# Kernel optimization log

Hardware: AMD Instinct MI355X
Metric: run time of the kernel (lower is better)

Reference implementation:

```python
import jax, jax.numpy as jnp
import numpy as np

B, S, D, H = 4, 4096, 2048, 512
EPS = 1e-5


def setup_inputs() -> dict:
    key = jax.random.key(0)
    ks = jax.random.split(key, 5)
    x = jax.random.normal(ks[0], (B, S, D), dtype=jnp.float32)
    ln_gamma = jnp.ones((D,), dtype=jnp.float32)
    ln_beta = jnp.zeros((D,), dtype=jnp.float32)
    # 'small' init: uniform in [1e-5 - 1e-6, 1e-5 + 1e-6]; use scaled randn here
    # so gradients are non-trivial, same math either way.
    W_down = jax.random.normal(ks[1], (H, D), dtype=jnp.float32) * 0.02
    b_down = jax.random.normal(ks[2], (H,), dtype=jnp.float32) * 0.02
    W_up = jax.random.normal(ks[3], (D, H), dtype=jnp.float32) * 0.02
    b_up = jax.random.normal(ks[4], (D,), dtype=jnp.float32) * 0.02
    return {"x": x, "ln_gamma": ln_gamma, "ln_beta": ln_beta,
            "W_down": W_down, "b_down": b_down, "W_up": W_up, "b_up": b_up}


def _layer_norm(x, gamma, beta):
    mu = jnp.mean(x, axis=-1, keepdims=True)
    var = jnp.mean(jnp.square(x - mu), axis=-1, keepdims=True)
    return (x - mu) * jax.lax.rsqrt(var + EPS) * gamma + beta


def reference(x, ln_gamma, ln_beta, W_down, b_down, W_up, b_up):
    # LayerNorm -> down-proj -> ReLU -> up-proj -> residual add
    y = _layer_norm(x, ln_gamma, ln_beta)                      # [B,S,D]
    y = jnp.einsum('bsd,hd->bsh', y, W_down) + b_down          # [B,S,H]
    y = jax.nn.relu(y)
    y = jnp.einsum('bsh,dh->bsd', y, W_up) + b_up              # [B,S,D]
    return x + y
```

## Files before the change

kernel.cpp:

```cpp
#include <hip/hip_runtime.h>

#define DD 2048
#define HH 512
#define NTOK 16384

typedef __attribute__((ext_vector_type(8))) short short8_t;
typedef __attribute__((ext_vector_type(4))) short short4_t;
typedef __attribute__((ext_vector_type(4))) float f32x4;

static __device__ __forceinline__ short f2bf(float f) {
    union { float f; unsigned u; } v; v.f = f;
    unsigned r = (v.u + 0x7fffu + ((v.u >> 16) & 1u)) >> 16;
    return (short)r;
}
static __device__ __forceinline__ float bf2f(unsigned short s) {
    union { unsigned u; float f; } v; v.u = (unsigned)s << 16;
    return v.f;
}

static __device__ __forceinline__ void gl16(const short* g, short* l) {
    __builtin_amdgcn_global_load_lds(
        (const __attribute__((address_space(1))) unsigned int*)g,
        (__attribute__((address_space(3))) unsigned int*)l, 16, 0, 0);
}

__global__ __launch_bounds__(256) void k_prep(
    const float* __restrict__ Wd, const float* __restrict__ g,
    const float* __restrict__ be, const float* __restrict__ Wu,
    const float* __restrict__ x,
    short* __restrict__ Wg, short* __restrict__ Wub,
    float* __restrict__ c2, short* __restrict__ xn,
    float* __restrict__ muv, float* __restrict__ sdv)
{
    __shared__ float ss[4], sq[4];
    int bid = blockIdx.x;
    int w = threadIdx.x >> 6, lane = threadIdx.x & 63;
    if (bid < 128) {
        int h = bid * 4 + w;
        const float* wr = Wd + (size_t)h * DD;
        float s2 = 0.f;
        for (int i = 0; i < 8; i++) {
            int col = i * 256 + lane * 4;
            float4 wv = *(const float4*)(wr + col);
            float4 gv = *(const float4*)(g + col);
            float4 bv = *(const float4*)(be + col);
            s2 += bv.x * wv.x + bv.y * wv.y + bv.z * wv.z + bv.w * wv.w;
            short4_t o;
            o[0] = f2bf(wv.x * gv.x); o[1] = f2bf(wv.y * gv.y);
            o[2] = f2bf(wv.z * gv.z); o[3] = f2bf(wv.w * gv.w);
            *(short4_t*)(Wg + (size_t)h * DD + col) = o;
        }
        for (int m = 1; m < 64; m <<= 1) s2 += __shfl_xor(s2, m);
        if (lane == 0) c2[h] = s2;
    } else if (bid < 384) {
        int b = bid - 128;
        for (int r = 0; r < 4; r++) {
            int i = (b * 4 + r) * 1024 + threadIdx.x * 4;
            float4 v = *(const float4*)(Wu + i);
            short4_t o;
            o[0] = f2bf(v.x); o[1] = f2bf(v.y); o[2] = f2bf(v.z); o[3] = f2bf(v.w);
            *(short4_t*)(Wub + i) = o;
        }
    } else {
        int row = bid - 384;
        const float* xr = x + (size_t)row * DD + threadIdx.x * 8;
        float4 a = *(const float4*)xr;
        float4 b = *(const float4*)(xr + 4);
        float s = a.x + a.y + a.z + a.w + b.x + b.y + b.z + b.w;
        float q = a.x * a.x + a.y * a.y + a.z * a.z + a.w * a.w
                + b.x * b.x + b.y * b.y + b.z * b.z + b.w * b.w;
        for (int m = 1; m < 64; m <<= 1) { s += __shfl_xor(s, m); q += __shfl_xor(q, m); }
        if (lane == 0) { ss[w] = s; sq[w] = q; }
        __syncthreads();
        float S = ss[0] + ss[1] + ss[2] + ss[3];
        float Q = sq[0] + sq[1] + sq[2] + sq[3];
        float mu = S * (1.f / DD);
        float ve = Q * (1.f / DD) - mu * mu + 1e-5f;
        float rs = rsqrtf(ve);
        if (threadIdx.x == 0) { muv[row] = mu; sdv[row] = ve * rs; }
        short8_t o;
        o[0] = f2bf((a.x - mu) * rs); o[1] = f2bf((a.y - mu) * rs);
        o[2] = f2bf((a.z - mu) * rs); o[3] = f2bf((a.w - mu) * rs);
        o[4] = f2bf((b.x - mu) * rs); o[5] = f2bf((b.y - mu) * rs);
        o[6] = f2bf((b.z - mu) * rs); o[7] = f2bf((b.w - mu) * rs);
        *(short8_t*)(xn + (size_t)row * DD + threadIdx.x * 8) = o;
    }
}

__global__ __launch_bounds__(256, 2) void k_down(
    const short* __restrict__ xn, const short* __restrict__ Wg,
    const float* __restrict__ c2, const float* __restrict__ bd,
    short* __restrict__ hid)
{
    __shared__ __align__(16) short sA[2][128 * 64];
    __shared__ __align__(16) short sB[2][128 * 64];

    int bid = blockIdx.x;
    int nb = (bid & 7) * 64 + (bid >> 3);
    const int m0 = (nb >> 2) * 128;
    const int n0 = (nb & 3) * 128;

    const int tid = threadIdx.x, lane = tid & 63, w = tid >> 6;
    const int l15 = lane & 15, rg = lane >> 4;
    const int wm = w >> 1, wn = w & 1;

    auto stage = [&](int b, int kb) {
#pragma unroll
        for (int i = 0; i < 4; i++) {
            int ch = i * 256 + tid;
            int r = ch >> 3, c = ch & 7;
            int co = ((c ^ (r & 7)) << 3);
            gl16(xn + (size_t)(m0 + r) * DD + kb + co,
                 &sA[b][0] + (i * 256 + (w << 6)) * 8);
            gl16(Wg + (size_t)(n0 + r) * DD + kb + co,
                 &sB[b][0] + (i * 256 + (w << 6)) * 8);
        }
    };

    f32x4 acc[4][4];
#pragma unroll
    for (int i = 0; i < 4; i++)
#pragma unroll
        for (int j = 0; j < 4; j++) acc[i][j] = (f32x4){0.f, 0.f, 0.f, 0.f};

    stage(0, 0);
    __syncthreads();

    for (int t = 0; t < 32; t++) {
        int cur = t & 1, nxt = cur ^ 1;
        if (t < 31) stage(nxt, (t + 1) * 64);
#pragma unroll
        for (int kk = 0; kk < 2; kk++) {
            int kc = kk * 4 + rg;
            short8_t af[4], bf[4];
#pragma unroll
            for (int mi = 0; mi < 4; mi++) {
                int rr = wm * 64 + mi * 16 + l15;
                af[mi] = *(const short8_t*)(&sA[cur][0] + rr * 64 + ((kc ^ (rr & 7)) << 3));
            }
#pragma unroll
            for (int ni = 0; ni < 4; ni++) {
                int rr = wn * 64 + ni * 16 + l15;
                bf[ni] = *(const short8_t*)(&sB[cur][0] + rr * 64 + ((kc ^ (rr & 7)) << 3));
            }
#pragma unroll
            for (int mi = 0; mi < 4; mi++)
#pragma unroll
                for (int ni = 0; ni < 4; ni++)
                    acc[mi][ni] = __builtin_amdgcn_mfma_f32_16x16x32_bf16(
                        af[mi], bf[ni], acc[mi][ni], 0, 0, 0);
        }
        __syncthreads();
    }

#pragma unroll
    for (int ni = 0; ni < 4; ni++) {
        int h = n0 + wn * 64 + ni * 16 + l15;
        float C = c2[h] + bd[h];
#pragma unroll
        for (int mi = 0; mi < 4; mi++) {
#pragma unroll
            for (int j = 0; j < 4; j++) {
                int rowL = wm * 64 + mi * 16 + rg * 4 + j;
                float v = acc[mi][ni][j] + C;
                v = v > 0.f ? v : 0.f;
                hid[(size_t)(m0 + rowL) * HH + h] = f2bf(v);
            }
        }
    }
}

__global__ __launch_bounds__(256, 2) void k_up(
    const short* __restrict__ xn, const short* __restrict__ hid,
    const short* __restrict__ Wub, const float* __restrict__ bu,
    const float* __restrict__ muv, const float* __restrict__ sdv,
    float* __restrict__ out)
{
    __shared__ __align__(16) short sA[2][128 * 64];
    __shared__ __align__(16) short sB[2][128 * 64];
    __shared__ float s_mu[128], s_sd[128];

    int bid = blockIdx.x;
    int nb = (bid & 7) * 256 + (bid >> 3);
    const int m0 = (nb >> 4) * 128;
    const int n0 = (nb & 15) * 128;

    const int tid = threadIdx.x, lane = tid & 63, w = tid >> 6;
    const int l15 = lane & 15, rg = lane >> 4;
    const int wm = w >> 1, wn = w & 1;

    auto stage = [&](int b, int kb) {
#pragma unroll
        for (int i = 0; i < 4; i++) {
            int ch = i * 256 + tid;
            int r = ch >> 3, c = ch & 7;
            int co = ((c ^ (r & 7)) << 3);
            gl16(hid + (size_t)(m0 + r) * HH + kb + co,
                 &sA[b][0] + (i * 256 + (w << 6)) * 8);
            gl16(Wub + (size_t)(n0 + r) * HH + kb + co,
                 &sB[b][0] + (i * 256 + (w << 6)) * 8);
        }
    };

    f32x4 acc[4][4];
#pragma unroll
    for (int i = 0; i < 4; i++)
#pragma unroll
        for (int j = 0; j < 4; j++) acc[i][j] = (f32x4){0.f, 0.f, 0.f, 0.f};

    stage(0, 0);
    if (tid < 128) { s_mu[tid] = muv[m0 + tid]; s_sd[tid] = sdv[m0 + tid]; }
    __syncthreads();

    for (int t = 0; t < 8; t++) {
        int cur = t & 1, nxt = cur ^ 1;
        if (t < 7) stage(nxt, (t + 1) * 64);
#pragma unroll
        for (int kk = 0; kk < 2; kk++) {
            int kc = kk * 4 + rg;
            short8_t af[4], bf[4];
#pragma unroll
            for (int mi = 0; mi < 4; mi++) {
                int rr = wm * 64 + mi * 16 + l15;
                af[mi] = *(const short8_t*)(&sA[cur][0] + rr * 64 + ((kc ^ (rr & 7)) << 3));
            }
#pragma unroll
            for (int ni = 0; ni < 4; ni++) {
                int rr = wn * 64 + ni * 16 + l15;
                bf[ni] = *(const short8_t*)(&sB[cur][0] + rr * 64 + ((kc ^ (rr & 7)) << 3));
            }
#pragma unroll
            for (int mi = 0; mi < 4; mi++)
#pragma unroll
                for (int ni = 0; ni < 4; ni++)
                    acc[mi][ni] = __builtin_amdgcn_mfma_f32_16x16x32_bf16(
                        af[mi], bf[ni], acc[mi][ni], 0, 0, 0);
        }
        __syncthreads();
    }

#pragma unroll
    for (int ni = 0; ni < 4; ni++) {
        int d = n0 + wn * 64 + ni * 16 + l15;
        float B = bu[d];
#pragma unroll
        for (int mi = 0; mi < 4; mi++) {
#pragma unroll
            for (int j = 0; j < 4; j++) {
                int rowL = wm * 64 + mi * 16 + rg * 4 + j;
                size_t idx = (size_t)(m0 + rowL) * DD + d;
                float xv = bf2f(((const unsigned short*)xn)[idx]);
                out[idx] = fmaf(xv, s_sd[rowL], s_mu[rowL]) + B + acc[mi][ni][j];
            }
        }
    }
}

extern "C" void kernel_launch(void* const* d_in, const int* in_sizes, int n_in,
                              void* d_out, int out_size, void* d_ws, size_t ws_size,
                              hipStream_t stream) {
    const float* x     = (const float*)d_in[0];
    const float* gamma = (const float*)d_in[1];
    const float* beta  = (const float*)d_in[2];
    const float* Wd_f  = (const float*)d_in[3];
    const float* bd    = (const float*)d_in[4];
    const float* Wu_f  = (const float*)d_in[5];
    const float* bu    = (const float*)d_in[6];

    short* Wg  = (short*)d_ws;
    short* Wub = Wg + (size_t)HH * DD;
    float* c2  = (float*)(Wub + (size_t)DD * HH);
    float* muv = c2 + HH;
    float* sdv = muv + NTOK;
    short* hid = (short*)(sdv + NTOK);
    short* xn  = hid + (size_t)NTOK * HH;

    k_prep<<<384 + NTOK, 256, 0, stream>>>(Wd_f, gamma, beta, Wu_f, x,
                                           Wg, Wub, c2, xn, muv, sdv);
    k_down<<<(NTOK / 128) * (HH / 128), 256, 0, stream>>>(xn, Wg, c2, bd, hid);
    k_up<<<(NTOK / 128) * (DD / 128), 256, 0, stream>>>(xn, hid, Wub, bu,
                                                        muv, sdv, (float*)d_out);
}
```

Before: 154.7 us.

## Shrink GEMM tiles to 128x64 for higher occupancy and stage k_up epilogue through LDS

Both GEMM kernels move from 128x128 to 128x64 tiles, with each wave taking 32 rows and a smaller accumulator. Launch bounds rise to 3 blocks per CU and the grids double. This targets occupancy and tail quantisation, at the cost of more global traffic for the A operand, since each A tile is now reused across half as many columns. The k_up epilogue now writes accumulators to swizzled LDS and then emits coalesced float4 stores with vectorised xn and bias loads, replacing strided scalar stores.

```diff
diff --git a/kernel.cpp b/kernel.cpp
--- a/kernel.cpp
+++ b/kernel.cpp
@@ -87,39 +87,44 @@
     }
 }
 
-__global__ __launch_bounds__(256, 2) void k_down(
+__global__ __launch_bounds__(256, 3) void k_down(
     const short* __restrict__ xn, const short* __restrict__ Wg,
     const float* __restrict__ c2, const float* __restrict__ bd,
     short* __restrict__ hid)
 {
-    __shared__ __align__(16) short sA[2][128 * 64];
-    __shared__ __align__(16) short sB[2][128 * 64];
+    __shared__ __align__(16) char smem[49152];
+    short* sA = (short*)smem;
+    short* sB = (short*)(smem + 32768);
 
     int bid = blockIdx.x;
-    int nb = (bid & 7) * 64 + (bid >> 3);
-    const int m0 = (nb >> 2) * 128;
-    const int n0 = (nb & 3) * 128;
+    int nb = (bid & 7) * 128 + (bid >> 3);
+    const int n0 = (nb & 7) * 64;
+    const int m0 = (nb >> 3) * 128;
 
     const int tid = threadIdx.x, lane = tid & 63, w = tid >> 6;
     const int l15 = lane & 15, rg = lane >> 4;
-    const int wm = w >> 1, wn = w & 1;
+    const int wm = w;
 
     auto stage = [&](int b, int kb) {
 #pragma unroll
         for (int i = 0; i < 4; i++) {
             int ch = i * 256 + tid;
             int r = ch >> 3, c = ch & 7;
-            int co = ((c ^ (r & 7)) << 3);
-            gl16(xn + (size_t)(m0 + r) * DD + kb + co,
-                 &sA[b][0] + (i * 256 + (w << 6)) * 8);
-            gl16(Wg + (size_t)(n0 + r) * DD + kb + co,
-                 &sB[b][0] + (i * 256 + (w << 6)) * 8);
+            gl16(xn + (size_t)(m0 + r) * DD + kb + ((c ^ (r & 7)) << 3),
+                 sA + b * 8192 + (i * 256 + (w << 6)) * 8);
+        }
+#pragma unroll
+        for (int i = 0; i < 2; i++) {
+            int ch = i * 256 + tid;
+            int r = ch >> 3, c = ch & 7;
+            gl16(Wg + (size_t)(n0 + r) * DD + kb + ((c ^ (r & 7)) << 3),
+                 sB + b * 4096 + (i * 256 + (w << 6)) * 8);
         }
     };
 
-    f32x4 acc[4][4];
-#pragma unroll
-    for (int i = 0; i < 4; i++)
+    f32x4 acc[2][4];
+#pragma unroll
+    for (int i = 0; i < 2; i++)
 #pragma unroll
         for (int j = 0; j < 4; j++) acc[i][j] = (f32x4){0.f, 0.f, 0.f, 0.f};
 
@@ -132,19 +137,19 @@
 #pragma unroll
         for (int kk = 0; kk < 2; kk++) {
             int kc = kk * 4 + rg;
-            short8_t af[4], bf[4];
-#pragma unroll
-            for (int mi = 0; mi < 4; mi++) {
-                int rr = wm * 64 + mi * 16 + l15;
-                af[mi] = *(const short8_t*)(&sA[cur][0] + rr * 64 + ((kc ^ (rr & 7)) << 3));
+            short8_t af[2], bf[4];
+#pragma unroll
+            for (int mi = 0; mi < 2; mi++) {
+                int rr = wm * 32 + mi * 16 + l15;
+                af[mi] = *(const short8_t*)(sA + cur * 8192 + rr * 64 + ((kc ^ (rr & 7)) << 3));
             }
 #pragma unroll
             for (int ni = 0; ni < 4; ni++) {
-                int rr = wn * 64 + ni * 16 + l15;
-                bf[ni] = *(const short8_t*)(&sB[cur][0] + rr * 64 + ((kc ^ (rr & 7)) << 3));
-            }
-#pragma unroll
-            for (int mi = 0; mi < 4; mi++)
+                int rr = ni * 16 + l15;
+                bf[ni] = *(const short8_t*)(sB + cur * 4096 + rr * 64 + ((kc ^ (rr & 7)) << 3));
+            }
+#pragma unroll
+            for (int mi = 0; mi < 2; mi++)
 #pragma unroll
                 for (int ni = 0; ni < 4; ni++)
                     acc[mi][ni] = __builtin_amdgcn_mfma_f32_16x16x32_bf16(
@@ -155,13 +160,13 @@
 
 #pragma unroll
     for (int ni = 0; ni < 4; ni++) {
-        int h = n0 + wn * 64 + ni * 16 + l15;
+        int h = n0 + ni * 16 + l15;
         float C = c2[h] + bd[h];
 #pragma unroll
-        for (int mi = 0; mi < 4; mi++) {
+        for (int mi = 0; mi < 2; mi++) {
 #pragma unroll
             for (int j = 0; j < 4; j++) {
-                int rowL = wm * 64 + mi * 16 + rg * 4 + j;
+                int rowL = wm * 32 + mi * 16 + rg * 4 + j;
                 float v = acc[mi][ni][j] + C;
                 v = v > 0.f ? v : 0.f;
                 hid[(size_t)(m0 + rowL) * HH + h] = f2bf(v);
@@ -170,41 +175,47 @@
     }
 }
 
-__global__ __launch_bounds__(256, 2) void k_up(
+__global__ __launch_bounds__(256, 3) void k_up(
     const short* __restrict__ xn, const short* __restrict__ hid,
     const short* __restrict__ Wub, const float* __restrict__ bu,
     const float* __restrict__ muv, const float* __restrict__ sdv,
     float* __restrict__ out)
 {
-    __shared__ __align__(16) short sA[2][128 * 64];
-    __shared__ __align__(16) short sB[2][128 * 64];
-    __shared__ float s_mu[128], s_sd[128];
+    __shared__ __align__(16) char smem[50176];
+    short* sA  = (short*)smem;
+    short* sB  = (short*)(smem + 32768);
+    float* s_mu = (float*)(smem + 49152);
+    float* s_sd = (float*)(smem + 49664);
 
     int bid = blockIdx.x;
-    int nb = (bid & 7) * 256 + (bid >> 3);
-    const int m0 = (nb >> 4) * 128;
-    const int n0 = (nb & 15) * 128;
+    int nb = (bid & 7) * 512 + (bid >> 3);
+    const int n0 = (nb & 31) * 64;
+    const int m0 = (nb >> 5) * 128;
 
     const int tid = threadIdx.x, lane = tid & 63, w = tid >> 6;
     const int l15 = lane & 15, rg = lane >> 4;
-    const int wm = w >> 1, wn = w & 1;
+    const int wm = w;
 
     auto stage = [&](int b, int kb) {
 #pragma unroll
         for (int i = 0; i < 4; i++) {
             int ch = i * 256 + tid;
             int r = ch >> 3, c = ch & 7;
-            int co = ((c ^ (r & 7)) << 3);
-            gl16(hid + (size_t)(m0 + r) * HH + kb + co,
-                 &sA[b][0] + (i * 256 + (w << 6)) * 8);
-            gl16(Wub + (size_t)(n0 + r) * HH + kb + co,
-                 &sB[b][0] + (i * 256 + (w << 6)) * 8);
+            gl16(hid + (size_t)(m0 + r) * HH + kb + ((c ^ (r & 7)) << 3),
+                 sA + b * 8192 + (i * 256 + (w << 6)) * 8);
+        }
+#pragma unroll
+        for (int i = 0; i < 2; i++) {
+            int ch = i * 256 + tid;
+            int r = ch >> 3, c = ch & 7;
+            gl16(Wub + (size_t)(n0 + r) * HH + kb + ((c ^ (r & 7)) << 3),
+                 sB + b * 4096 + (i * 256 + (w << 6)) * 8);
         }
     };
 
-    f32x4 acc[4][4];
-#pragma unroll
-    for (int i = 0; i < 4; i++)
+    f32x4 acc[2][4];
+#pragma unroll
+    for (int i = 0; i < 2; i++)
 #pragma unroll
         for (int j = 0; j < 4; j++) acc[i][j] = (f32x4){0.f, 0.f, 0.f, 0.f};
 
@@ -218,19 +229,19 @@
 #pragma unroll
         for (int kk = 0; kk < 2; kk++) {
             int kc = kk * 4 + rg;
-            short8_t af[4], bf[4];
-#pragma unroll
-            for (int mi = 0; mi < 4; mi++) {
-                int rr = wm * 64 + mi * 16 + l15;
-                af[mi] = *(const short8_t*)(&sA[cur][0] + rr * 64 + ((kc ^ (rr & 7)) << 3));
+            short8_t af[2], bf[4];
+#pragma unroll
+            for (int mi = 0; mi < 2; mi++) {
+                int rr = wm * 32 + mi * 16 + l15;
+                af[mi] = *(const short8_t*)(sA + cur * 8192 + rr * 64 + ((kc ^ (rr & 7)) << 3));
             }
 #pragma unroll
             for (int ni = 0; ni < 4; ni++) {
-                int rr = wn * 64 + ni * 16 + l15;
-                bf[ni] = *(const short8_t*)(&sB[cur][0] + rr * 64 + ((kc ^ (rr & 7)) << 3));
-            }
-#pragma unroll
-            for (int mi = 0; mi < 4; mi++)
+                int rr = ni * 16 + l15;
+                bf[ni] = *(const short8_t*)(sB + cur * 4096 + rr * 64 + ((kc ^ (rr & 7)) << 3));
+            }
+#pragma unroll
+            for (int mi = 0; mi < 2; mi++)
 #pragma unroll
                 for (int ni = 0; ni < 4; ni++)
                     acc[mi][ni] = __builtin_amdgcn_mfma_f32_16x16x32_bf16(
@@ -239,19 +250,35 @@
         __syncthreads();
     }
 
-#pragma unroll
-    for (int ni = 0; ni < 4; ni++) {
-        int d = n0 + wn * 64 + ni * 16 + l15;
-        float B = bu[d];
-#pragma unroll
-        for (int mi = 0; mi < 4; mi++) {
+    float* C = (float*)smem;
+#pragma unroll
+    for (int ni = 0; ni < 4; ni++)
+#pragma unroll
+        for (int mi = 0; mi < 2; mi++)
 #pragma unroll
             for (int j = 0; j < 4; j++) {
-                int rowL = wm * 64 + mi * 16 + rg * 4 + j;
-                size_t idx = (size_t)(m0 + rowL) * DD + d;
-                float xv = bf2f(((const unsigned short*)xn)[idx]);
-                out[idx] = fmaf(xv, s_sd[rowL], s_mu[rowL]) + B + acc[mi][ni][j];
-            }
+                int row = wm * 32 + mi * 16 + rg * 4 + j;
+                int colsw = (ni * 16 + l15) ^ ((row & 7) << 2);
+                C[row * 64 + colsw] = acc[mi][ni][j];
+            }
+    __syncthreads();
+
+    {
+        const int row = tid >> 1, half = tid & 1, r7 = row & 7;
+        const float mu = s_mu[row], sd = s_sd[row];
+        const size_t rb = (size_t)(m0 + row) * DD + n0 + half * 32;
+        const float* burow = bu + n0 + half * 32;
+#pragma unroll
+        for (int i = 0; i < 8; i++) {
+            f32x4 c = *(const f32x4*)&C[row * 64 + half * 32 + 4 * (i ^ r7)];
+            short4_t xv = *(const short4_t*)(xn + rb + i * 4);
+            float4 bv = *(const float4*)(burow + i * 4);
+            f32x4 o;
+            o[0] = fmaf(bf2f((unsigned short)xv[0]), sd, mu) + bv.x + c[0];
+            o[1] = fmaf(bf2f((unsigned short)xv[1]), sd, mu) + bv.y + c[1];
+            o[2] = fmaf(bf2f((unsigned short)xv[2]), sd, mu) + bv.z + c[2];
+            o[3] = fmaf(bf2f((unsigned short)xv[3]), sd, mu) + bv.w + c[3];
+            *(f32x4*)&out[rb + i * 4] = o;
         }
     }
 }
@@ -277,7 +304,7 @@
 
     k_prep<<<384 + NTOK, 256, 0, stream>>>(Wd_f, gamma, beta, Wu_f, x,
                                            Wg, Wub, c2, xn, muv, sdv);
-    k_down<<<(NTOK / 128) * (HH / 128), 256, 0, stream>>>(xn, Wg, c2, bd, hid);
-    k_up<<<(NTOK / 128) * (DD / 128), 256, 0, stream>>>(xn, hid, Wub, bu,
-                                                        muv, sdv, (float*)d_out);
-}
+    k_down<<<(NTOK / 128) * (HH / 64), 256, 0, stream>>>(xn, Wg, c2, bd, hid);
+    k_up<<<(NTOK / 128) * (DD / 64), 256, 0, stream>>>(xn, hid, Wub, bu,
+                                                       muv, sdv, (float*)d_out);
+}
```

New measurement: 176.3 us. 14.0% more time.
